# Performance work log

Hardware: AMD Instinct MI355X
Metric: run time of the kernel (lower is better)

The kernel has to match this reference:

```python
import jax, jax.numpy as jnp
import numpy as np

CONTEXT_SIZE = 32
NDIM = 64
HEAD_SIZE = 64
BATCH = 16384


def setup_inputs() -> dict:
    key = jax.random.key(0)
    kx, kk, kq, kv = jax.random.split(key, 4)
    x = jax.random.normal(kx, (BATCH, CONTEXT_SIZE, NDIM), dtype=jnp.float32)
    # nn.Linear(ndim, head_size, bias=False): y = x @ W.T, W is [head_size, ndim].
    # We store transposed weights [ndim, head_size] so y = x @ W.
    scale = 1.0 / np.sqrt(NDIM)
    Wk = jax.random.normal(kk, (NDIM, HEAD_SIZE), dtype=jnp.float32) * scale
    Wq = jax.random.normal(kq, (NDIM, HEAD_SIZE), dtype=jnp.float32) * scale
    Wv = jax.random.normal(kv, (NDIM, HEAD_SIZE), dtype=jnp.float32) * scale
    return {"x": x, "Wk": Wk, "Wq": Wq, "Wv": Wv}


def reference(x, Wk, Wq, Wv):
    # x: [B, T, D] with T == CONTEXT_SIZE
    k = x @ Wk  # [B, T, H]
    q = x @ Wq  # [B, T, H]
    v = x @ Wv  # [B, T, H]
    # Faithful to source: p = q @ k^T / head_size**(-0.5) == q @ k^T * sqrt(head_size)
    p = jnp.einsum("bth,bsh->bts", q, k) * jnp.sqrt(jnp.float32(HEAD_SIZE))
    causal = jnp.tril(jnp.ones((CONTEXT_SIZE, CONTEXT_SIZE), dtype=bool))
    p = jnp.where(causal, p, -jnp.inf)
    p = jax.nn.softmax(p, axis=-1)
    # dropout is identity in eval mode
    return jnp.einsum("bts,bsh->bth", p, v)  # [B, T, H]
```

## Files before the change

kernel.cpp:

```cpp
#include <hip/hip_runtime.h>
#include <hip/hip_bf16.h>

typedef __attribute__((ext_vector_type(8))) short short8;
typedef __attribute__((ext_vector_type(4))) float f32x4;
typedef __attribute__((ext_vector_type(2))) unsigned int u32x2;
typedef __attribute__((ext_vector_type(4))) unsigned int u32x4;

#define CTX 32
#define ND  64
#define NH  64
#define LOG2E_8 11.541560327111707f
#define NB_PER_WAVE 2

#define OFF_MH 0
#define OFF_ML 8192
#define OFF_WAVE 16384
#define PWSTR 80
#define PW_RTH 0
#define PW_RTL 2560
#define PW_VT  0
#define PW_P   5120
#define WAVE_BYTES 7680
#define LDS_BYTES (OFF_WAVE + 4 * WAVE_BYTES)

__device__ __forceinline__ unsigned short f2bf(float f) {
  unsigned int u = __builtin_bit_cast(unsigned int, f);
  u += 0x7FFFu + ((u >> 16) & 1u);
  return (unsigned short)(u >> 16);
}
__device__ __forceinline__ float bf2f(unsigned short b) {
  unsigned int u = ((unsigned int)b) << 16;
  return __builtin_bit_cast(float, u);
}
__device__ __forceinline__ unsigned int pkrn(float a, float b) {
  const __hip_bfloat162 t = __float22bfloat162_rn(make_float2(a, b));
  unsigned int u;
  __builtin_memcpy(&u, &t, 4);
  return u;
}
__device__ __forceinline__ float2 unpk(unsigned int w) {
  __hip_bfloat162 t;
  __builtin_memcpy(&t, &w, 4);
  return __bfloat1622float2(t);
}

#define MFMA(a, b, c) __builtin_amdgcn_mfma_f32_16x16x32_bf16((a), (b), (c), 0, 0, 0)

__global__ __launch_bounds__(256) void mk_m(
    const float* __restrict__ Wq, const float* __restrict__ Wk,
    const float* __restrict__ Wv,
    unsigned short* __restrict__ MtH, unsigned short* __restrict__ MtL,
    unsigned short* __restrict__ WvT)
{
  const int idx = blockIdx.x * 256 + threadIdx.x;
  const int dp = idx >> 6, d = idx & 63;
  const float* wq = Wq + d * 64;
  const float* wk = Wk + dp * 64;
  float acc = 0.f;
  #pragma unroll
  for (int h = 0; h < 64; ++h) acc = fmaf(wq[h], wk[h], acc);
  acc *= LOG2E_8;
  const unsigned short hi = f2bf(acc);
  MtH[idx] = hi;
  MtL[idx] = f2bf(acc - bf2f(hi));
  WvT[idx] = f2bf(Wv[d * 64 + dp]);
}

struct Batch {
  short8 xh[2][2], xl[2][2];
  f32x4  pa[2][2];
  char*  wl;
  float* ob;
};

__device__ __forceinline__ void load_x(const float* __restrict__ xb,
                                       f32x4 (&xr)[2][2][2], int c, int g) {
  #pragma unroll
  for (int mt = 0; mt < 2; ++mt)
    #pragma unroll
    for (int kt = 0; kt < 2; ++kt) {
      const float* p = xb + (16 * mt + c) * ND + 32 * kt + 8 * g;
      xr[mt][kt][0] = *(const f32x4*)(p);
      xr[mt][kt][1] = *(const f32x4*)(p + 4);
    }
}

__device__ __forceinline__ void split8(const f32x4 a0, const f32x4 a1,
                                       short8& hi, short8& lo) {
  u32x4 hw, lw;
  #pragma unroll
  for (int w = 0; w < 2; ++w) {
    {
      const float x0 = a0[2 * w], x1 = a0[2 * w + 1];
      const unsigned int h = pkrn(x0, x1);
      const float2 hf = unpk(h);
      hw[w] = h;
      lw[w] = pkrn(x0 - hf.x, x1 - hf.y);
    }
    {
      const float x0 = a1[2 * w], x1 = a1[2 * w + 1];
      const unsigned int h = pkrn(x0, x1);
      const float2 hf = unpk(h);
      hw[2 + w] = h;
      lw[2 + w] = pkrn(x0 - hf.x, x1 - hf.y);
    }
  }
  hi = __builtin_bit_cast(short8, hw);
  lo = __builtin_bit_cast(short8, lw);
}

__device__ __forceinline__ void split_x(Batch& s, const f32x4 (&xr)[2][2][2]) {
  #pragma unroll
  for (int mt = 0; mt < 2; ++mt)
    #pragma unroll
    for (int kt = 0; kt < 2; ++kt)
      split8(xr[mt][kt][0], xr[mt][kt][1], s.xh[mt][kt], s.xl[mt][kt]);
  #pragma unroll
  for (int i = 0; i < 2; ++i)
    #pragma unroll
    for (int j = 0; j < 2; ++j) s.pa[i][j] = f32x4{0.f, 0.f, 0.f, 0.f};
}

__device__ __forceinline__ void qk_fill(Batch& s, const char* lds,
                                        int kt, int ntl, int c, int g) {
  const int nt = 2 * kt + ntl;
  f32x4 a0 = {0.f, 0.f, 0.f, 0.f};
  f32x4 a1 = {0.f, 0.f, 0.f, 0.f};
  #pragma unroll
  for (int kk = 0; kk < 2; ++kk) {
    const int row = 16 * nt + c;
    const int byte = row * 128 + ((64 * kk + 16 * g) ^ ((row & 7) << 4));
    const short8 bh = *(const short8*)(lds + OFF_MH + byte);
    const short8 bl = *(const short8*)(lds + OFF_ML + byte);
    a0 = MFMA(s.xh[0][kk], bh, a0);
    a0 = MFMA(s.xh[0][kk], bl, a0);
    a0 = MFMA(s.xl[0][kk], bh, a0);
    a1 = MFMA(s.xh[1][kk], bh, a1);
    a1 = MFMA(s.xh[1][kk], bl, a1);
    a1 = MFMA(s.xl[1][kk], bh, a1);
  }
  const int col2 = 2 * (16 * ntl + c);
  #pragma unroll
  for (int pr = 0; pr < 2; ++pr) {
    {
      const unsigned int h = pkrn(a0[2 * pr], a0[2 * pr + 1]);
      const float2 hf = unpk(h);
      const unsigned int l = pkrn(a0[2 * pr] - hf.x, a0[2 * pr + 1] - hf.y);
      const int rb = (4 * g + 2 * pr) * PWSTR + col2;
      *(unsigned short*)(s.wl + PW_RTH + rb)         = (unsigned short)h;
      *(unsigned short*)(s.wl + PW_RTH + rb + PWSTR) = (unsigned short)(h >> 16);
      *(unsigned short*)(s.wl + PW_RTL + rb)         = (unsigned short)l;
      *(unsigned short*)(s.wl + PW_RTL + rb + PWSTR) = (unsigned short)(l >> 16);
    }
    {
      const unsigned int h = pkrn(a1[2 * pr], a1[2 * pr + 1]);
      const float2 hf = unpk(h);
      const unsigned int l = pkrn(a1[2 * pr] - hf.x, a1[2 * pr + 1] - hf.y);
      const int rb = (16 + 4 * g + 2 * pr) * PWSTR + col2;
      *(unsigned short*)(s.wl + PW_RTH + rb)         = (unsigned short)h;
      *(unsigned short*)(s.wl + PW_RTH + rb + PWSTR) = (unsigned short)(h >> 16);
      *(unsigned short*)(s.wl + PW_RTL + rb)         = (unsigned short)l;
      *(unsigned short*)(s.wl + PW_RTL + rb + PWSTR) = (unsigned short)(l >> 16);
    }
  }
}

__device__ __forceinline__ void qk_consume(Batch& s, int kt, int c, int g) {
  short8 tH[2], tL[2];
  #pragma unroll
  for (int i = 0; i < 2; ++i) {
    const int off = (16 * i + c) * PWSTR + 16 * g;
    tH[i] = *(const short8*)(s.wl + PW_RTH + off);
    tL[i] = *(const short8*)(s.wl + PW_RTL + off);
  }
  #pragma unroll
  for (int mt = 0; mt < 2; ++mt)
    #pragma unroll
    for (int nt2 = 0; nt2 < 2; ++nt2) {
      s.pa[mt][nt2] = MFMA(s.xh[mt][kt], tH[nt2], s.pa[mt][nt2]);
      s.pa[mt][nt2] = MFMA(s.xl[mt][kt], tH[nt2], s.pa[mt][nt2]);
      s.pa[mt][nt2] = MFMA(s.xh[mt][kt], tL[nt2], s.pa[mt][nt2]);
    }
}

__device__ __forceinline__ void softmax_store(Batch& s, int c, int g) {
  char* const pbuf = s.wl + PW_P;
  #pragma unroll
  for (int nt = 0; nt < 2; ++nt) {
    const int t = 16 * nt + c;
    float v[8];
    #pragma unroll
    for (int mt = 0; mt < 2; ++mt)
      #pragma unroll
      for (int j = 0; j < 4; ++j) {
        const int sidx = 16 * mt + 4 * g + j;
        v[4 * mt + j] = (sidx <= t) ? s.pa[mt][nt][j] : -__builtin_inff();
      }
    float m = fmaxf(fmaxf(fmaxf(v[0], v[1]), fmaxf(v[2], v[3])),
                    fmaxf(fmaxf(v[4], v[5]), fmaxf(v[6], v[7])));
    m = fmaxf(m, __shfl_xor(m, 16));
    m = fmaxf(m, __shfl_xor(m, 32));
    float e[8], ssum = 0.f;
    #pragma unroll
    for (int i = 0; i < 8; ++i) { e[i] = exp2f(v[i] - m); ssum += e[i]; }
    ssum += __shfl_xor(ssum, 16);
    ssum += __shfl_xor(ssum, 32);
    const float r = __builtin_amdgcn_rcpf(ssum);
    #pragma unroll
    for (int mt = 0; mt < 2; ++mt) {
      const u32x2 w2 = {pkrn(e[4 * mt] * r, e[4 * mt + 1] * r),
                        pkrn(e[4 * mt + 2] * r, e[4 * mt + 3] * r)};
      *(u32x2*)(pbuf + t * PWSTR + 32 * mt + 8 * g) = w2;
    }
  }
}

__device__ __forceinline__ void vproj(Batch& s, const short8 (&bvr)[4][2],
                                      int c, int g) {
  #pragma unroll
  for (int nt = 0; nt < 4; ++nt) {
    f32x4 a0 = {0.f, 0.f, 0.f, 0.f};
    f32x4 a1 = {0.f, 0.f, 0.f, 0.f};
    #pragma unroll
    for (int kk = 0; kk < 2; ++kk) {
      a0 = MFMA(s.xh[0][kk], bvr[nt][kk], a0);
      a1 = MFMA(s.xh[1][kk], bvr[nt][kk], a1);
    }
    char* const vrow = s.wl + PW_VT + (16 * nt + c) * PWSTR;
    const u32x2 w0 = {pkrn(a0[0], a0[1]), pkrn(a0[2], a0[3])};
    const u32x2 w1 = {pkrn(a1[0], a1[1]), pkrn(a1[2], a1[3])};
    *(u32x2*)(vrow + 8 * g)      = w0;
    *(u32x2*)(vrow + 32 + 8 * g) = w1;
  }
}

__device__ __forceinline__ void pv_store(Batch& s, int c, int g) {
  char* const pbuf = s.wl + PW_P;
  const short8 ap0 = *(const short8*)(pbuf + c * PWSTR + 16 * g);
  const short8 ap1 = *(const short8*)(pbuf + (16 + c) * PWSTR + 16 * g);
  #pragma unroll
  for (int mh = 0; mh < 4; ++mh) {
    const short8 bv = *(const short8*)(s.wl + PW_VT + (16 * mh + c) * PWSTR + 16 * g);
    f32x4 o0 = {0.f, 0.f, 0.f, 0.f};
    f32x4 o1 = {0.f, 0.f, 0.f, 0.f};
    o0 = MFMA(bv, ap0, o0);
    o1 = MFMA(bv, ap1, o1);
    *(f32x4*)(s.ob + c * NH + 16 * mh + 4 * g)        = o0;
    *(f32x4*)(s.ob + (16 + c) * NH + 16 * mh + 4 * g) = o1;
  }
}

__global__ __launch_bounds__(256, 3) void head_fused(
    const float* __restrict__ x,
    const unsigned short* __restrict__ MtH, const unsigned short* __restrict__ MtL,
    const unsigned short* __restrict__ WvT,
    float* __restrict__ out, int wstride)
{
  __shared__ __align__(16) char lds[LDS_BYTES];
  const int tid = threadIdx.x;

  {
    const unsigned int* srcH = (const unsigned int*)MtH;
    const unsigned int* srcL = (const unsigned int*)MtL;
    #pragma unroll
    for (int i = 0; i < 8; ++i) {
      const int e = tid + 256 * i;
      const int row = e >> 5;
      const int byte = row * 128 + (((e & 31) * 4) ^ ((row & 7) << 4));
      *(unsigned int*)(lds + OFF_MH + byte) = srcH[e];
      *(unsigned int*)(lds + OFF_ML + byte) = srcL[e];
    }
  }
  __syncthreads();

  const int wid  = tid >> 6;
  const int lane = tid & 63;
  const int c = lane & 15;
  const int g = lane >> 4;

  short8 bvr[4][2];
  #pragma unroll
  for (int nt = 0; nt < 4; ++nt)
    #pragma unroll
    for (int kk = 0; kk < 2; ++kk)
      bvr[nt][kk] = *(const short8*)(WvT + (16 * nt + c) * 64 + 32 * kk + 8 * g);

  Batch S;
  S.wl = lds + OFF_WAVE + wid * WAVE_BYTES;

  const int w = blockIdx.x * 4 + wid;

  f32x4 xc[2][2][2], xn[2][2][2];
  load_x(x + (long)w * (CTX * ND), xc, c, g);

  #pragma unroll
  for (int it = 0; it < NB_PER_WAVE; ++it) {
    const long b = (long)w + (long)it * wstride;
    if (it + 1 < NB_PER_WAVE)
      load_x(x + (b + wstride) * (CTX * ND), xn, c, g);
    S.ob = out + b * (CTX * NH);
    split_x(S, xc);
    #pragma unroll
    for (int kt = 0; kt < 2; ++kt) {
      qk_fill(S, lds, kt, 0, c, g);
      qk_fill(S, lds, kt, 1, c, g);
      qk_consume(S, kt, c, g);
    }
    softmax_store(S, c, g);
    vproj(S, bvr, c, g);
    pv_store(S, c, g);
    if (it + 1 < NB_PER_WAVE) {
      #pragma unroll
      for (int i = 0; i < 2; ++i)
        #pragma unroll
        for (int k = 0; k < 2; ++k)
          #pragma unroll
          for (int h = 0; h < 2; ++h) xc[i][k][h] = xn[i][k][h];
    }
  }
}

extern "C" void kernel_launch(void* const* d_in, const int* in_sizes, int n_in,
                              void* d_out, int out_size, void* d_ws, size_t ws_size,
                              hipStream_t stream) {
  const float* x  = (const float*)d_in[0];
  const float* Wk = (const float*)d_in[1];
  const float* Wq = (const float*)d_in[2];
  const float* Wv = (const float*)d_in[3];
  float* out = (float*)d_out;

  unsigned short* MtH = (unsigned short*)d_ws;
  unsigned short* MtL = MtH + 64 * 64;
  unsigned short* WvT = MtL + 64 * 64;

  mk_m<<<dim3(16), dim3(256), 0, stream>>>(Wq, Wk, Wv, MtH, MtL, WvT);

  const int batch = in_sizes[0] / (CTX * ND);
  const int wstride = batch / NB_PER_WAVE;
  head_fused<<<dim3(wstride / 4), dim3(256), 0, stream>>>(x, MtH, MtL, WvT, out, wstride);
}
```

Baseline: 59.64 us.

## Compute V projection early in registers and defer softmax normalization to output

The V projection MFMAs now run right after the x split and keep their packed bf16 results in registers, so they can overlap the QK phase. The results are written to LDS only after QK finishes. Softmax now stores unnormalized exponentials and applies the reciprocal row sum to the PV output accumulator, which takes the multiply off the path before the P store. This raises register pressure under launch_bounds(256,3) and slightly changes rounding, because unnormalized probabilities are packed to bf16.

New measurement: 62.82 us. 1.05x slower.

```diff
diff --git a/kernel.cpp b/kernel.cpp
--- a/kernel.cpp
+++ b/kernel.cpp
@@ -121,6 +121,32 @@
     for (int j = 0; j < 2; ++j) s.pa[i][j] = f32x4{0.f, 0.f, 0.f, 0.f};
 }
 
+__device__ __forceinline__ void vproj_reg(Batch& s, const short8 (&bvr)[4][2],
+                                          u32x2 (&vpk)[4][2]) {
+  #pragma unroll
+  for (int nt = 0; nt < 4; ++nt) {
+    f32x4 a0 = {0.f, 0.f, 0.f, 0.f};
+    f32x4 a1 = {0.f, 0.f, 0.f, 0.f};
+    #pragma unroll
+    for (int kk = 0; kk < 2; ++kk) {
+      a0 = MFMA(s.xh[0][kk], bvr[nt][kk], a0);
+      a1 = MFMA(s.xh[1][kk], bvr[nt][kk], a1);
+    }
+    vpk[nt][0] = u32x2{pkrn(a0[0], a0[1]), pkrn(a0[2], a0[3])};
+    vpk[nt][1] = u32x2{pkrn(a1[0], a1[1]), pkrn(a1[2], a1[3])};
+  }
+}
+
+__device__ __forceinline__ void vt_write(Batch& s, const u32x2 (&vpk)[4][2],
+                                         int c, int g) {
+  #pragma unroll
+  for (int nt = 0; nt < 4; ++nt) {
+    char* const vrow = s.wl + PW_VT + (16 * nt + c) * PWSTR;
+    *(u32x2*)(vrow + 8 * g)      = vpk[nt][0];
+    *(u32x2*)(vrow + 32 + 8 * g) = vpk[nt][1];
+  }
+}
+
 __device__ __forceinline__ void qk_fill(Batch& s, const char* lds,
                                         int kt, int ntl, int c, int g) {
   const int nt = 2 * kt + ntl;
@@ -183,8 +209,10 @@
     }
 }
 
-__device__ __forceinline__ void softmax_store(Batch& s, int c, int g) {
+__device__ __forceinline__ void softmax_store(Batch& s, int c, int g,
+                                              float& r0, float& r1) {
   char* const pbuf = s.wl + PW_P;
+  float rr[2];
   #pragma unroll
   for (int nt = 0; nt < 2; ++nt) {
     const int t = 16 * nt + c;
@@ -200,41 +228,26 @@
                     fmaxf(fmaxf(v[4], v[5]), fmaxf(v[6], v[7])));
     m = fmaxf(m, __shfl_xor(m, 16));
     m = fmaxf(m, __shfl_xor(m, 32));
-    float e[8], ssum = 0.f;
-    #pragma unroll
-    for (int i = 0; i < 8; ++i) { e[i] = exp2f(v[i] - m); ssum += e[i]; }
+    float e[8];
+    #pragma unroll
+    for (int i = 0; i < 8; ++i) e[i] = exp2f(v[i] - m);
+    #pragma unroll
+    for (int mt = 0; mt < 2; ++mt) {
+      const u32x2 w2 = {pkrn(e[4 * mt], e[4 * mt + 1]),
+                        pkrn(e[4 * mt + 2], e[4 * mt + 3])};
+      *(u32x2*)(pbuf + t * PWSTR + 32 * mt + 8 * g) = w2;
+    }
+    float ssum = ((e[0] + e[1]) + (e[2] + e[3])) + ((e[4] + e[5]) + (e[6] + e[7]));
     ssum += __shfl_xor(ssum, 16);
     ssum += __shfl_xor(ssum, 32);
-    const float r = __builtin_amdgcn_rcpf(ssum);
-    #pragma unroll
-    for (int mt = 0; mt < 2; ++mt) {
-      const u32x2 w2 = {pkrn(e[4 * mt] * r, e[4 * mt + 1] * r),
-                        pkrn(e[4 * mt + 2] * r, e[4 * mt + 3] * r)};
-      *(u32x2*)(pbuf + t * PWSTR + 32 * mt + 8 * g) = w2;
-    }
-  }
-}
-
-__device__ __forceinline__ void vproj(Batch& s, const short8 (&bvr)[4][2],
-                                      int c, int g) {
-  #pragma unroll
-  for (int nt = 0; nt < 4; ++nt) {
-    f32x4 a0 = {0.f, 0.f, 0.f, 0.f};
-    f32x4 a1 = {0.f, 0.f, 0.f, 0.f};
-    #pragma unroll
-    for (int kk = 0; kk < 2; ++kk) {
-      a0 = MFMA(s.xh[0][kk], bvr[nt][kk], a0);
-      a1 = MFMA(s.xh[1][kk], bvr[nt][kk], a1);
-    }
-    char* const vrow = s.wl + PW_VT + (16 * nt + c) * PWSTR;
-    const u32x2 w0 = {pkrn(a0[0], a0[1]), pkrn(a0[2], a0[3])};
-    const u32x2 w1 = {pkrn(a1[0], a1[1]), pkrn(a1[2], a1[3])};
-    *(u32x2*)(vrow + 8 * g)      = w0;
-    *(u32x2*)(vrow + 32 + 8 * g) = w1;
-  }
-}
-
-__device__ __forceinline__ void pv_store(Batch& s, int c, int g) {
+    rr[nt] = __builtin_amdgcn_rcpf(ssum);
+  }
+  r0 = rr[0];
+  r1 = rr[1];
+}
+
+__device__ __forceinline__ void pv_store(Batch& s, float r0, float r1,
+                                         int c, int g) {
   char* const pbuf = s.wl + PW_P;
   const short8 ap0 = *(const short8*)(pbuf + c * PWSTR + 16 * g);
   const short8 ap1 = *(const short8*)(pbuf + (16 + c) * PWSTR + 16 * g);
@@ -245,6 +258,8 @@
     f32x4 o1 = {0.f, 0.f, 0.f, 0.f};
     o0 = MFMA(bv, ap0, o0);
     o1 = MFMA(bv, ap1, o1);
+    o0 *= r0;
+    o1 *= r1;
     *(f32x4*)(s.ob + c * NH + 16 * mh + 4 * g)        = o0;
     *(f32x4*)(s.ob + (16 + c) * NH + 16 * mh + 4 * g) = o1;
   }
@@ -300,15 +315,18 @@
       load_x(x + (b + wstride) * (CTX * ND), xn, c, g);
     S.ob = out + b * (CTX * NH);
     split_x(S, xc);
+    u32x2 vpk[4][2];
+    vproj_reg(S, bvr, vpk);
     #pragma unroll
     for (int kt = 0; kt < 2; ++kt) {
       qk_fill(S, lds, kt, 0, c, g);
       qk_fill(S, lds, kt, 1, c, g);
       qk_consume(S, kt, c, g);
     }
-    softmax_store(S, c, g);
-    vproj(S, bvr, c, g);
-    pv_store(S, c, g);
+    vt_write(S, vpk, c, g);
+    float r0, r1;
+    softmax_store(S, c, g, r0, r1);
+    pv_store(S, r0, r1, c, g);
     if (it + 1 < NB_PER_WAVE) {
       #pragma unroll
       for (int i = 0; i < 2; ++i)
```
